# Kernel tuning notes

Hardware: AMD Instinct MI355X
Metric: run time of the kernel (lower is better)

The kernel has to match this reference:

```python
import jax, jax.numpy as jnp
import numpy as np

B, S, E, H = 2, 2048, 1024, 16
DH = E // H  # 64
EPS = 1e-5


def layer_norm(x, g, b):
    mu = jnp.mean(x, axis=-1, keepdims=True)
    var = jnp.mean(jnp.square(x - mu), axis=-1, keepdims=True)
    return (x - mu) * jax.lax.rsqrt(var + EPS) * g + b


def setup_inputs() -> dict:
    key = jax.random.key(0)
    ks = jax.random.split(key, 12)
    s = lambda fan_in: 1.0 / np.sqrt(fan_in)
    return {
        "x": jax.random.normal(ks[0], (B, S, E), dtype=jnp.float32),
        "ln1_g": jnp.ones((E,), jnp.float32),
        "ln1_b": jnp.zeros((E,), jnp.float32),
        # per-head projections, batched over head axis: [H, E, DH]
        "Wq": jax.random.uniform(ks[1], (H, E, DH), jnp.float32, -s(E), s(E)),
        "Wk": jax.random.uniform(ks[2], (H, E, DH), jnp.float32, -s(E), s(E)),
        "Wv": jax.random.uniform(ks[3], (H, E, DH), jnp.float32, -s(E), s(E)),
        "Wo": jax.random.uniform(ks[4], (H * DH, E), jnp.float32, -s(H * DH), s(H * DH)),
        "bo": jax.random.uniform(ks[5], (E,), jnp.float32, -s(H * DH), s(H * DH)),
        "ln2_g": jnp.ones((E,), jnp.float32),
        "ln2_b": jnp.zeros((E,), jnp.float32),
        "W1": jax.random.uniform(ks[6], (E, 4 * E), jnp.float32, -s(E), s(E)),
        "b1": jax.random.uniform(ks[7], (4 * E,), jnp.float32, -s(E), s(E)),
        "W2": jax.random.uniform(ks[8], (4 * E, E), jnp.float32, -s(4 * E), s(4 * E)),
        "b2": jax.random.uniform(ks[9], (E,), jnp.float32, -s(4 * E), s(4 * E)),
    }


def reference(x, ln1_g, ln1_b, Wq, Wk, Wv, Wo, bo, ln2_g, ln2_b, W1, b1, W2, b2):
    b, s, e = x.shape
    # --- multi-head attention (pre-LN) ---
    h = layer_norm(x, ln1_g, ln1_b)
    q = jnp.einsum("bse,hed->bhsd", h, Wq)
    k = jnp.einsum("bse,hed->bhsd", h, Wk)
    v = jnp.einsum("bse,hed->bhsd", h, Wv)
    # NOTE: original scales by channel**-0.5 (embed_size), not head_size
    scores = jnp.einsum("bhsd,bhtd->bhst", q, k) * (e ** -0.5)
    causal = jnp.tril(jnp.ones((s, s), dtype=bool))
    scores = jnp.where(causal, scores, -jnp.inf)
    attn = jax.nn.softmax(scores, axis=-1)  # dropout is identity in eval
    out = jnp.einsum("bhst,bhtd->bhsd", attn, v)
    out = out.transpose(0, 2, 1, 3).reshape(b, s, -1)  # concat heads: [B,S,H*DH]
    x = x + out @ Wo + bo
    # --- feed-forward (pre-LN) ---
    h2 = layer_norm(x, ln2_g, ln2_b)
    ff = jax.nn.relu(h2 @ W1 + b1) @ W2 + b2
    return x + ff
```

## Files before the change

### kernel.cpp

```cpp
#include <hip/hip_runtime.h>


typedef __bf16 bf16_t;
typedef __attribute__((ext_vector_type(8))) __bf16 bf16x8;
typedef __attribute__((ext_vector_type(4))) __bf16 bf16x4;
typedef __attribute__((ext_vector_type(4))) float f32x4;

#define B_DIM 2
#define S_DIM 2048
#define E_DIM 1024
#define H_DIM 16
#define DH_DIM 64

#define GLD16(gp, lp) __builtin_amdgcn_global_load_lds( \
    (const __attribute__((address_space(1))) void*)(gp), \
    (__attribute__((address_space(3))) void*)(lp), 16, 0, 0)

#define Q_SCALE 0.0450842120f

__global__ __launch_bounds__(256) void ln_kernel(
    const float* __restrict__ x, const float* __restrict__ g,
    const float* __restrict__ bv, bf16_t* __restrict__ out)
{
  const int row = blockIdx.x;
  const int t = threadIdx.x;
  const float* xr = x + (size_t)row * E_DIM;
  float4 v = *(const float4*)&xr[t * 4];
  float s  = v.x + v.y + v.z + v.w;
  float s2 = v.x*v.x + v.y*v.y + v.z*v.z + v.w*v.w;
#pragma unroll
  for (int m = 1; m < 64; m <<= 1) {
    s  += __shfl_xor(s,  m, 64);
    s2 += __shfl_xor(s2, m, 64);
  }
  __shared__ float red[8];
  const int wid = t >> 6, lane = t & 63;
  if (lane == 0) { red[wid] = s; red[4 + wid] = s2; }
  __syncthreads();
  s  = red[0] + red[1] + red[2] + red[3];
  s2 = red[4] + red[5] + red[6] + red[7];
  const float mu  = s * (1.f / E_DIM);
  const float var = s2 * (1.f / E_DIM) - mu * mu;
  const float rs  = rsqrtf(var + 1e-5f);
  float4 gg = *(const float4*)&g[t * 4];
  float4 bb = *(const float4*)&bv[t * 4];
  bf16x4 o;
  o[0] = (bf16_t)((v.x - mu) * rs * gg.x + bb.x);
  o[1] = (bf16_t)((v.y - mu) * rs * gg.y + bb.y);
  o[2] = (bf16_t)((v.z - mu) * rs * gg.z + bb.z);
  o[3] = (bf16_t)((v.w - mu) * rs * gg.w + bb.w);
  *(bf16x4*)&out[(size_t)row * E_DIM + t * 4] = o;
}

__global__ __launch_bounds__(256) void reduce2_ln(
    const bf16_t* __restrict__ p0, const bf16_t* __restrict__ p1,
    const float* __restrict__ bo, const float* __restrict__ x,
    const float* __restrict__ g, const float* __restrict__ bv,
    float* __restrict__ xmid, bf16_t* __restrict__ h2)
{
  const int row = blockIdx.x;
  const int t = threadIdx.x;
  const size_t off = (size_t)row * E_DIM + t * 4;
  bf16x4 a = *(const bf16x4*)&p0[off];
  bf16x4 b4 = *(const bf16x4*)&p1[off];
  float4 xr = *(const float4*)&x[off];
  float4 bo4 = *(const float4*)&bo[t * 4];
  float4 v;
  v.x = (float)a[0] + (float)b4[0] + xr.x + bo4.x;
  v.y = (float)a[1] + (float)b4[1] + xr.y + bo4.y;
  v.z = (float)a[2] + (float)b4[2] + xr.z + bo4.z;
  v.w = (float)a[3] + (float)b4[3] + xr.w + bo4.w;
  *(float4*)&xmid[off] = v;
  float s  = v.x + v.y + v.z + v.w;
  float s2 = v.x*v.x + v.y*v.y + v.z*v.z + v.w*v.w;
#pragma unroll
  for (int m = 1; m < 64; m <<= 1) {
    s  += __shfl_xor(s,  m, 64);
    s2 += __shfl_xor(s2, m, 64);
  }
  __shared__ float red[8];
  const int wid = t >> 6, lane = t & 63;
  if (lane == 0) { red[wid] = s; red[4 + wid] = s2; }
  __syncthreads();
  s  = red[0] + red[1] + red[2] + red[3];
  s2 = red[4] + red[5] + red[6] + red[7];
  const float mu  = s * (1.f / E_DIM);
  const float var = s2 * (1.f / E_DIM) - mu * mu;
  const float rs  = rsqrtf(var + 1e-5f);
  float4 gg = *(const float4*)&g[t * 4];
  float4 bb = *(const float4*)&bv[t * 4];
  bf16x4 o;
  o[0] = (bf16_t)((v.x - mu) * rs * gg.x + bb.x);
  o[1] = (bf16_t)((v.y - mu) * rs * gg.y + bb.y);
  o[2] = (bf16_t)((v.z - mu) * rs * gg.z + bb.z);
  o[3] = (bf16_t)((v.w - mu) * rs * gg.w + bb.w);
  *(bf16x4*)&h2[off] = o;
}

__global__ __launch_bounds__(256) void reduce4(
    const bf16_t* __restrict__ p0, const bf16_t* __restrict__ p1,
    const bf16_t* __restrict__ p2, const bf16_t* __restrict__ p3,
    const float* __restrict__ b2, const float* __restrict__ xm,
    float* __restrict__ out)
{
  const int row = blockIdx.x;
  const int t = threadIdx.x;
  const size_t off = (size_t)row * E_DIM + t * 4;
  bf16x4 a0 = *(const bf16x4*)&p0[off];
  bf16x4 a1 = *(const bf16x4*)&p1[off];
  bf16x4 a2 = *(const bf16x4*)&p2[off];
  bf16x4 a3 = *(const bf16x4*)&p3[off];
  float4 xr = *(const float4*)&xm[off];
  float4 bb = *(const float4*)&b2[t * 4];
  float4 o;
  o.x = (float)a0[0] + (float)a1[0] + (float)a2[0] + (float)a3[0] + xr.x + bb.x;
  o.y = (float)a0[1] + (float)a1[1] + (float)a2[1] + (float)a3[1] + xr.y + bb.y;
  o.z = (float)a0[2] + (float)a1[2] + (float)a2[2] + (float)a3[2] + xr.z + bb.z;
  o.w = (float)a0[3] + (float)a1[3] + (float)a2[3] + (float)a3[3] + xr.w + bb.w;
  *(float4*)&out[off] = o;
}

__global__ __launch_bounds__(256) void pack_weights(
    const float* __restrict__ Wq, const float* __restrict__ Wk,
    const float* __restrict__ Wv, bf16_t* __restrict__ WqkvT,
    const float* __restrict__ Wo, bf16_t* __restrict__ WoT,
    const float* __restrict__ W1, bf16_t* __restrict__ W1T,
    const float* __restrict__ W2, bf16_t* __restrict__ W2T)
{
  __shared__ float tile[64][65];
  const int bid = blockIdx.x;
  const int t = threadIdx.x;
  const int rr = t >> 2;

  if (bid < 768) {
    const int byq = bid >> 4, bxq = bid & 15;
    const int m = byq >> 4, h = byq & 15;
    const float* src = (m == 0 ? Wq : (m == 1 ? Wk : Wv)) + (size_t)h * E_DIM * DH_DIM;
    const int e0 = bxq * 64;
#pragma unroll
    for (int u = 0; u < 4; u++) {
      const int cc = (t & 3) * 4 + u * 16;
      float4 f = *(const float4*)&src[(size_t)(e0 + rr) * DH_DIM + cc];
      tile[rr][cc + 0] = f.x; tile[rr][cc + 1] = f.y;
      tile[rr][cc + 2] = f.z; tile[rr][cc + 3] = f.w;
    }
    __syncthreads();
    const int oc = t >> 2;
    const size_t drow = (size_t)(m * 1024 + h * 64 + oc) * E_DIM;
#pragma unroll
    for (int u = 0; u < 4; u++) {
      const int orr = (t & 3) * 4 + u * 16;
      bf16x4 w;
      w[0] = (bf16_t)tile[orr + 0][oc];
      w[1] = (bf16_t)tile[orr + 1][oc];
      w[2] = (bf16_t)tile[orr + 2][oc];
      w[3] = (bf16_t)tile[orr + 3][oc];
      *(bf16x4*)&WqkvT[drow + e0 + orr] = w;
    }
    return;
  }

  const float* src; bf16_t* dst; int R, C, bx, by;
  if (bid < 1024)      { const int r = bid - 768;  src = Wo; dst = WoT; R = 1024; C = 1024; bx = r & 15; by = r >> 4; }
  else if (bid < 2048) { const int r = bid - 1024; src = W1; dst = W1T; R = 1024; C = 4096; bx = r & 63; by = r >> 6; }
  else                 { const int r = bid - 2048; src = W2; dst = W2T; R = 4096; C = 1024; bx = r & 15; by = r >> 4; }
  const int c0 = bx * 64, r0 = by * 64;
#pragma unroll
  for (int u = 0; u < 4; u++) {
    const int cc = (t & 3) * 4 + u * 16;
    float4 f = *(const float4*)&src[(size_t)(r0 + rr) * C + c0 + cc];
    tile[rr][cc + 0] = f.x; tile[rr][cc + 1] = f.y;
    tile[rr][cc + 2] = f.z; tile[rr][cc + 3] = f.w;
  }
  __syncthreads();
  const int oc = t >> 2;
#pragma unroll
  for (int u = 0; u < 4; u++) {
    const int orr = (t & 3) * 4 + u * 16;
    bf16x4 w;
    w[0] = (bf16_t)tile[orr + 0][oc];
    w[1] = (bf16_t)tile[orr + 1][oc];
    w[2] = (bf16_t)tile[orr + 2][oc];
    w[3] = (bf16_t)tile[orr + 3][oc];
    *(bf16x4*)&dst[(size_t)(c0 + oc) * R + r0 + orr] = w;
  }
}

constexpr int EPI_QKV = 0, EPI_BIAS_RELU = 2, EPI_PART_F32 = 3, EPI_PART_B16 = 4;


template <int EPI>
__global__ __launch_bounds__(256) void gemm128_kernel(
    const bf16_t* __restrict__ A, const bf16_t* __restrict__ Bt,
    int M, int N, int Kst, int Klen, int RM, int RN,
    const float* __restrict__ bias,
    float* __restrict__ outF, bf16_t* __restrict__ outB,
    bf16_t* __restrict__ qo, bf16_t* __restrict__ ko, bf16_t* __restrict__ vo)
{
  __shared__ bf16_t As[2][128 * 64];
  __shared__ bf16_t Bs[2][128 * 64];
  const int gx = gridDim.x;
  const int lin = blockIdx.y * gx + blockIdx.x;
  const int xcd = lin & 7, kb = lin >> 3;
  const int nregx = gx / RM;
  const int rx = xcd % nregx, ry = xcd / nregx;
  const int m0 = (rx * RM + kb % RM) * 128;
  const int n0 = (ry * RN + kb / RM) * 128;
  const int sp = blockIdx.z;
  A  += (size_t)sp * Klen;
  Bt += (size_t)sp * Klen;

  const int tid = threadIdx.x, lane = tid & 63, wid = tid >> 6;
  const int wr = wid >> 1, wc = wid & 1;
  const int lr = lane & 15, lg = lane >> 4;
  const int l7 = lr & 7;
  const int sl[2] = { (lg ^ l7) * 16, ((4 | lg) ^ l7) * 16 };
  const int rbA = (wr * 64 + lr) * 128;
  const int rbB = (wc * 64 + lr) * 128;

  auto stage = [&](int kt, int buf) {
#pragma unroll
    for (int q = 0; q < 4; q++) {
      const int L = q * 256 + tid;
      const int row = L >> 3;
      const int u = (L & 7) ^ (row & 7);
      char* la = (char*)&As[buf][0] + (size_t)(q * 256 + wid * 64) * 16;
      char* lb = (char*)&Bs[buf][0] + (size_t)(q * 256 + wid * 64) * 16;
      GLD16(A  + (size_t)(m0 + row) * Kst + kt * 64 + u * 8, la);
      GLD16(Bt + (size_t)(n0 + row) * Kst + kt * 64 + u * 8, lb);
    }
  };

  const f32x4 z4 = {0.f, 0.f, 0.f, 0.f};
  f32x4 acc[4][4];
#pragma unroll
  for (int i = 0; i < 4; i++)
#pragma unroll
    for (int j = 0; j < 4; j++) acc[i][j] = z4;

  const int NT = Klen / 64;
  stage(0, 0);
  for (int T = 0; T < NT; ++T) {
    const int b = T & 1;
    asm volatile("s_waitcnt vmcnt(0)" ::: "memory");
    __builtin_amdgcn_s_barrier();
    if (T + 1 < NT) stage(T + 1, b ^ 1);
    __builtin_amdgcn_sched_barrier(0);

    bf16x8 bfr[2][4];
#pragma unroll
    for (int kk = 0; kk < 2; kk++)
#pragma unroll
      for (int j = 0; j < 4; j++)
        bfr[kk][j] = *(const bf16x8*)((const char*)&Bs[b][0] + rbB + j * 2048 + sl[kk]);
    __builtin_amdgcn_s_setprio(1);
#pragma unroll
    for (int i = 0; i < 4; i++) {
#pragma unroll
      for (int kk = 0; kk < 2; kk++) {
        bf16x8 af = *(const bf16x8*)((const char*)&As[b][0] + rbA + i * 2048 + sl[kk]);
#pragma unroll
        for (int j = 0; j < 4; j++)
          acc[i][j] = __builtin_amdgcn_mfma_f32_16x16x32_bf16(af, bfr[kk][j], acc[i][j], 0, 0, 0);
      }
    }
    __builtin_amdgcn_s_setprio(0);
  }

#pragma unroll
  for (int i = 0; i < 4; i++) {
#pragma unroll
    for (int j = 0; j < 4; j++) {
#pragma unroll
      for (int r = 0; r < 4; r++) {
        const int m = m0 + wr * 64 + i * 16 + lg * 4 + r;
        const int n = n0 + wc * 64 + j * 16 + lr;
        const float val = acc[i][j][r];
        if constexpr (EPI == EPI_QKV) {
          const int tsel = n >> 10, h = (n >> 6) & 15, d = n & 63;
          const int b_ = m >> 11, s_ = m & 2047;
          if (tsel == 0)
            qo[((size_t)((b_ * H_DIM + h) * S_DIM + s_)) * DH_DIM + d] = (bf16_t)(val * Q_SCALE);
          else if (tsel == 1)
            ko[((size_t)((b_ * H_DIM + h) * S_DIM + s_)) * DH_DIM + d] = (bf16_t)val;
          else
            vo[((size_t)((b_ * H_DIM + h) * DH_DIM + d)) * S_DIM + s_] = (bf16_t)val;
        } else if constexpr (EPI == EPI_BIAS_RELU) {
          const float u = val + bias[n];
          outB[(size_t)m * N + n] = (bf16_t)(u > 0.f ? u : 0.f);
        } else if constexpr (EPI == EPI_PART_F32) {
          outF[(size_t)sp * M * N + (size_t)m * N + n] = val;
        } else {
          bf16_t* o = sp == 0 ? outB : sp == 1 ? qo : sp == 2 ? ko : vo;
          o[(size_t)m * N + n] = (bf16_t)val;
        }
      }
    }
  }
}

template <int EPI>
__global__ __launch_bounds__(512) void gemm256_kernel(
    const bf16_t* __restrict__ A, const bf16_t* __restrict__ Bt,
    int M, int N, int Kst, int Klen, int RM, int RN,
    const float* __restrict__ bias,
    float* __restrict__ outF, bf16_t* __restrict__ outB,
    bf16_t* __restrict__ qo, bf16_t* __restrict__ ko, bf16_t* __restrict__ vo)
{
  __shared__ bf16_t As[2][256 * 64];
  __shared__ bf16_t Bs[2][256 * 64];
  const int gx = gridDim.x;
  const int lin = blockIdx.y * gx + blockIdx.x;
  const int xcd = lin & 7, kb = lin >> 3;
  const int nregx = gx / RM;
  const int rx = xcd % nregx, ry = xcd / nregx;
  const int m0 = (rx * RM + kb % RM) * 256;
  const int n0 = (ry * RN + kb / RM) * 256;
  const int sp = blockIdx.z;
  A  += (size_t)sp * Klen;
  Bt += (size_t)sp * Klen;

  const int tid = threadIdx.x, lane = tid & 63, wid = tid >> 6;
  const int wm = wid >> 2, wn = wid & 3;
  const int lr = lane & 15, lg = lane >> 4;
  const int l7 = lr & 7;
  const int sl[2] = { (lg ^ l7) * 16, ((4 | lg) ^ l7) * 16 };
  const int rbA = (wm * 128 + lr) * 128;
  const int rbB = (wn * 64 + lr) * 128;

  auto stage = [&](int kt, int buf) {
#pragma unroll
    for (int q = 0; q < 4; q++) {
      const int L = q * 512 + tid;
      const int row = L >> 3;
      const int u = (L & 7) ^ (row & 7);
      char* la = (char*)&As[buf][0] + (size_t)(q * 512 + wid * 64) * 16;
      char* lb = (char*)&Bs[buf][0] + (size_t)(q * 512 + wid * 64) * 16;
      GLD16(A  + (size_t)(m0 + row) * Kst + kt * 64 + u * 8, la);
      GLD16(Bt + (size_t)(n0 + row) * Kst + kt * 64 + u * 8, lb);
    }
  };

  const f32x4 z4 = {0.f, 0.f, 0.f, 0.f};
  f32x4 acc[8][4];
#pragma unroll
  for (int i = 0; i < 8; i++)
#pragma unroll
    for (int j = 0; j < 4; j++) acc[i][j] = z4;

  const int NT = Klen / 64;
  stage(0, 0);
  for (int T = 0; T < NT; ++T) {
    const int b = T & 1;
    asm volatile("s_waitcnt vmcnt(0)" ::: "memory");
    __builtin_amdgcn_s_barrier();
    if (T + 1 < NT) stage(T + 1, b ^ 1);
    __builtin_amdgcn_sched_barrier(0);

    bf16x8 bfr[2][4];
#pragma unroll
    for (int kk = 0; kk < 2; kk++)
#pragma unroll
      for (int j = 0; j < 4; j++)
        bfr[kk][j] = *(const bf16x8*)((const char*)&Bs[b][0] + rbB + j * 2048 + sl[kk]);
    __builtin_amdgcn_s_setprio(1);
#pragma unroll
    for (int i = 0; i < 8; i++) {
#pragma unroll
      for (int kk = 0; kk < 2; kk++) {
        bf16x8 af = *(const bf16x8*)((const char*)&As[b][0] + rbA + i * 2048 + sl[kk]);
#pragma unroll
        for (int j = 0; j < 4; j++)
          acc[i][j] = __builtin_amdgcn_mfma_f32_16x16x32_bf16(af, bfr[kk][j], acc[i][j], 0, 0, 0);
      }
    }
    __builtin_amdgcn_s_setprio(0);
  }

#pragma unroll
  for (int i = 0; i < 8; i++) {
#pragma unroll
    for (int j = 0; j < 4; j++) {
#pragma unroll
      for (int r = 0; r < 4; r++) {
        const int m = m0 + wm * 128 + i * 16 + lg * 4 + r;
        const int n = n0 + wn * 64 + j * 16 + lr;
        const float val = acc[i][j][r];
        if constexpr (EPI == EPI_BIAS_RELU) {
          const float u = val + bias[n];
          outB[(size_t)m * N + n] = (bf16_t)(u > 0.f ? u : 0.f);
        } else if constexpr (EPI == EPI_PART_F32) {
          outF[(size_t)sp * M * N + (size_t)m * N + n] = val;
        } else if constexpr (EPI == EPI_PART_B16) {
          bf16_t* o = sp == 0 ? outB : sp == 1 ? qo : sp == 2 ? ko : vo;
          o[(size_t)m * N + n] = (bf16_t)val;
        }
      }
    }
  }
}

__global__ __launch_bounds__(256) void attn_kernel(
    const bf16_t* __restrict__ Q, const bf16_t* __restrict__ K,
    const bf16_t* __restrict__ Vt, bf16_t* __restrict__ O,
    bf16_t* __restrict__ Opart, float* __restrict__ mpart, float* __restrict__ lpart)
{
  __shared__ bf16_t Ks[2][64 * 64];
  __shared__ bf16_t Vs[2][64 * 64];
  __shared__ bf16_t Ps[4][2][16 * 64];

  const int nwg = 51 * gridDim.y;
  int id = blockIdx.y * 51 + blockIdx.x;
  id = (id & 7) * (nwg >> 3) + (id >> 3);
  const int bx = id % 51, bh = id / 51;

  int g = 0;
  while (3 * (g + 1) * (g + 2) / 2 <= bx) g++;
  const int rr_ = bx - 3 * g * (g + 1) / 2;
  const int q2 = 3 * g + rr_ / (g + 1);
  const int sp = rr_ % (g + 1);
  const int ns = g + 1;
  const int n2 = 2 * q2 + 2;
  const int lo = 6 * sp;
  const int hi = (6 * sp + 6 < n2) ? 6 * sp + 6 : n2;

  const int tid = threadIdx.x;
  const int wid = tid >> 6, lane = tid & 63;
  const int lr = lane & 15, lg = lane >> 4;
  const int q0w = q2 * 128 + wid * 32;

  const bf16_t* Qp = Q  + (size_t)bh * S_DIM * DH_DIM;
  const bf16_t* Kp = K  + (size_t)bh * S_DIM * DH_DIM;
  const bf16_t* Vp = Vt + (size_t)bh * DH_DIM * S_DIM;

  bf16x8 bq0[2], bq1[2];
#pragma unroll
  for (int c = 0; c < 2; c++) {
    bq0[c] = *(const bf16x8*)&Qp[(size_t)(q0w + lr) * DH_DIM + c * 32 + lg * 8];
    bq1[c] = *(const bf16x8*)&Qp[(size_t)(q0w + 16 + lr) * DH_DIM + c * 32 + lg * 8];
  }

  const f32x4 z4 = {0.f, 0.f, 0.f, 0.f};
  f32x4 Ot0[4], Ot1[4];
#pragma unroll
  for (int dt = 0; dt < 4; dt++) { Ot0[dt] = z4; Ot1[dt] = z4; }
  float mrow0 = -1e30f, lrow0 = 0.f;
  float mrow1 = -1e30f, lrow1 = 0.f;

  const int ktr = wid * 8 + (lane >> 3);
  const int ksc = lane & 7;

  auto stageKV = [&](int t0, int buf) {
#pragma unroll
    for (int p = 0; p < 2; p++) {
      const int tr = p * 32 + ktr;
      GLD16(Kp + (size_t)(t0 + tr) * DH_DIM + (ksc ^ (tr & 7)) * 8,
            &Ks[buf][(p * 32 + wid * 8) * 64]);
      GLD16(Vp + (size_t)tr * S_DIM + t0 + (ksc ^ (tr & 7)) * 8,
            &Vs[buf][(p * 32 + wid * 8) * 64]);
    }
  };

  stageKV(lo * 64, 0);

  for (int tc = lo; tc < hi; ++tc) {
    const int cur = (tc - lo) & 1;
    __syncthreads();
    if (tc + 1 < hi) stageKV((tc + 1) * 64, cur ^ 1);

    const int t0 = tc * 64;
    f32x4 s0[4], s1[4];
    __builtin_amdgcn_s_setprio(1);
#pragma unroll
    for (int j = 0; j < 4; j++) {
      f32x4 a = z4, b = z4;
      const int t = j * 16 + lr;
#pragma unroll
      for (int c = 0; c < 2; c++) {
        const int kbyte = t * 128 + (((c * 4 + lg) * 16) ^ ((t & 7) << 4));
        bf16x8 ak = *(const bf16x8*)((const char*)&Ks[cur][0] + kbyte);
        a = __builtin_amdgcn_mfma_f32_16x16x32_bf16(ak, bq0[c], a, 0, 0, 0);
        b = __builtin_amdgcn_mfma_f32_16x16x32_bf16(ak, bq1[c], b, 0, 0, 0);
      }
      s0[j] = a; s1[j] = b;
    }
    __builtin_amdgcn_s_setprio(0);
    if (tc >= 2 * q2) {
#pragma unroll
      for (int j = 0; j < 4; j++)
#pragma unroll
        for (int r = 0; r < 4; r++) {
          const int tg = t0 + j * 16 + lg * 4 + r;
          if (tg > q0w + lr)      s0[j][r] = -1e30f;
          if (tg > q0w + 16 + lr) s1[j][r] = -1e30f;
        }
    }
    {
      float mj[4];
#pragma unroll
      for (int j = 0; j < 4; j++)
        mj[j] = fmaxf(fmaxf(s0[j][0], s0[j][1]), fmaxf(s0[j][2], s0[j][3]));
      float tmax = fmaxf(fmaxf(mj[0], mj[1]), fmaxf(mj[2], mj[3]));
      tmax = fmaxf(tmax, __shfl_xor(tmax, 16, 64));
      tmax = fmaxf(tmax, __shfl_xor(tmax, 32, 64));
      if (!__all(tmax <= mrow0 + 8.f)) {
        const float mnew = fmaxf(mrow0, tmax);
        const float fsc = __builtin_exp2f(mrow0 - mnew);
        mrow0 = mnew; lrow0 *= fsc;
#pragma unroll
        for (int dt = 0; dt < 4; dt++)
#pragma unroll
          for (int r = 0; r < 4; r++) Ot0[dt][r] *= fsc;
      }
      float sj[4];
#pragma unroll
      for (int j = 0; j < 4; j++) {
#pragma unroll
        for (int r = 0; r < 4; r++) s0[j][r] = __builtin_exp2f(s0[j][r] - mrow0);
        sj[j] = (s0[j][0] + s0[j][1]) + (s0[j][2] + s0[j][3]);
      }
      float tsum = (sj[0] + sj[1]) + (sj[2] + sj[3]);
      tsum += __shfl_xor(tsum, 16, 64);
      tsum += __shfl_xor(tsum, 32, 64);
      lrow0 += tsum;
#pragma unroll
      for (int j = 0; j < 4; j++) {
        bf16x4 w;
#pragma unroll
        for (int r = 0; r < 4; r++) w[r] = (bf16_t)s0[j][r];
        const int pbyte = lr * 128 + ((j * 32 + lg * 8) ^ ((lr & 7) << 4));
        *(bf16x4*)((char*)&Ps[wid][0][0] + pbyte) = w;
      }
    }
    {
      float mj[4];
#pragma unroll
      for (int j = 0; j < 4; j++)
        mj[j] = fmaxf(fmaxf(s1[j][0], s1[j][1]), fmaxf(s1[j][2], s1[j][3]));
      float tmax = fmaxf(fmaxf(mj[0], mj[1]), fmaxf(mj[2], mj[3]));
      tmax = fmaxf(tmax, __shfl_xor(tmax, 16, 64));
      tmax = fmaxf(tmax, __shfl_xor(tmax, 32, 64));
      if (!__all(tmax <= mrow1 + 8.f)) {
        const float mnew = fmaxf(mrow1, tmax);
        const float fsc = __builtin_exp2f(mrow1 - mnew);
        mrow1 = mnew; lrow1 *= fsc;
#pragma unroll
        for (int dt = 0; dt < 4; dt++)
#pragma unroll
          for (int r = 0; r < 4; r++) Ot1[dt][r] *= fsc;
      }
      float sj[4];
#pragma unroll
      for (int j = 0; j < 4; j++) {
#pragma unroll
        for (int r = 0; r < 4; r++) s1[j][r] = __builtin_exp2f(s1[j][r] - mrow1);
        sj[j] = (s1[j][0] + s1[j][1]) + (s1[j][2] + s1[j][3]);
      }
      float tsum = (sj[0] + sj[1]) + (sj[2] + sj[3]);
      tsum += __shfl_xor(tsum, 16, 64);
      tsum += __shfl_xor(tsum, 32, 64);
      lrow1 += tsum;
#pragma unroll
      for (int j = 0; j < 4; j++) {
        bf16x4 w;
#pragma unroll
        for (int r = 0; r < 4; r++) w[r] = (bf16_t)s1[j][r];
        const int pbyte = lr * 128 + ((j * 32 + lg * 8) ^ ((lr & 7) << 4));
        *(bf16x4*)((char*)&Ps[wid][1][0] + pbyte) = w;
      }
    }

    __builtin_amdgcn_s_setprio(1);
#pragma unroll
    for (int c = 0; c < 2; c++) {
      const int abyte = lr * 128 + ((c * 64 + lg * 16) ^ ((lr & 7) << 4));
      bf16x8 pa0 = *(const bf16x8*)((const char*)&Ps[wid][0][0] + abyte);
      bf16x8 pa1 = *(const bf16x8*)((const char*)&Ps[wid][1][0] + abyte);
#pragma unroll
      for (int dt = 0; dt < 4; dt++) {
        const int d = dt * 16 + lr;
        const int vbyte = d * 128 + (((c * 4 + lg) * 16) ^ ((d & 7) << 4));
        bf16x8 bv = *(const bf16x8*)((const char*)&Vs[cur][0] + vbyte);
        Ot0[dt] = __builtin_amdgcn_mfma_f32_16x16x32_bf16(bv, pa0, Ot0[dt], 0, 0, 0);
        Ot1[dt] = __builtin_amdgcn_mfma_f32_16x16x32_bf16(bv, pa1, Ot1[dt], 0, 0, 0);
      }
    }
    __builtin_amdgcn_s_setprio(0);
  }

  if (ns == 1) {
    const int b = bh >> 4, h = bh & 15;
    {
      const float linv = 1.f / lrow0;
      const size_t base = ((size_t)(b * S_DIM + q0w + lr)) * E_DIM + h * DH_DIM;
#pragma unroll
      for (int dt = 0; dt < 4; dt++) {
        bf16x4 w;
#pragma unroll
        for (int r = 0; r < 4; r++) w[r] = (bf16_t)(Ot0[dt][r] * linv);
        *(bf16x4*)&O[base + dt * 16 + lg * 4] = w;
      }
    }
    {
      const float linv = 1.f / lrow1;
      const size_t base = ((size_t)(b * S_DIM + q0w + 16 + lr)) * E_DIM + h * DH_DIM;
#pragma unroll
      for (int dt = 0; dt < 4; dt++) {
        bf16x4 w;
#pragma unroll
        for (int r = 0; r < 4; r++) w[r] = (bf16_t)(Ot1[dt][r] * linv);
        *(bf16x4*)&O[base + dt * 16 + lg * 4] = w;
      }
    }
  } else {
    const int psl = bh * 48 + (bx - 3);
    bf16_t* Ob = Opart + (size_t)psl * 128 * 64;
    const int row0 = wid * 32 + lr, row1 = row0 + 16;
#pragma unroll
    for (int dt = 0; dt < 4; dt++) {
      bf16x4 w0, w1;
#pragma unroll
      for (int r = 0; r < 4; r++) { w0[r] = (bf16_t)Ot0[dt][r]; w1[r] = (bf16_t)Ot1[dt][r]; }
      *(bf16x4*)&Ob[row0 * 64 + dt * 16 + lg * 4] = w0;
      *(bf16x4*)&Ob[row1 * 64 + dt * 16 + lg * 4] = w1;
    }
    if (lg == 0) {
      mpart[psl * 128 + row0] = mrow0;
      lpart[psl * 128 + row0] = lrow0;
      mpart[psl * 128 + row1] = mrow1;
      lpart[psl * 128 + row1] = lrow1;
    }
  }
}

__global__ __launch_bounds__(256) void attn_combine(
    const bf16_t* __restrict__ Opart, const float* __restrict__ mpart,
    const float* __restrict__ lpart, bf16_t* __restrict__ O)
{
  const int q2 = 3 + (blockIdx.x >> 1);
  const int half = blockIdx.x & 1;
  const int bh = blockIdx.y;
  const int g = q2 / 3, ns = g + 1;
  const int sbase = 3 * g * (g + 1) / 2 + (q2 - 3 * g) * (g + 1) - 3;
  const int psl0 = bh * 48 + sbase;
  const int tid = threadIdx.x;
  const int q = tid >> 2, d0 = (tid & 3) * 16;
  const int row = half * 64 + q;

  float M = -1e30f;
  for (int s = 0; s < ns; s++) M = fmaxf(M, mpart[(psl0 + s) * 128 + row]);
  float L = 0.f;
  float acc[16];
#pragma unroll
  for (int j = 0; j < 16; j++) acc[j] = 0.f;
  for (int s = 0; s < ns; s++) {
    const float w = __builtin_exp2f(mpart[(psl0 + s) * 128 + row] - M);
    L += w * lpart[(psl0 + s) * 128 + row];
    const bf16_t* Ob = Opart + ((size_t)(psl0 + s) * 128 + row) * 64 + d0;
    bf16x8 o0 = *(const bf16x8*)Ob;
    bf16x8 o1 = *(const bf16x8*)(Ob + 8);
#pragma unroll
    for (int j = 0; j < 8; j++) { acc[j] += w * (float)o0[j]; acc[8 + j] += w * (float)o1[j]; }
  }
  const float inv = 1.f / L;
  const int b = bh >> 4, h = bh & 15;
  const int srow = q2 * 128 + row;
  bf16_t* out = O + ((size_t)(b * S_DIM + srow)) * E_DIM + h * DH_DIM + d0;
  bf16x8 w0, w1;
#pragma unroll
  for (int j = 0; j < 8; j++) { w0[j] = (bf16_t)(acc[j] * inv); w1[j] = (bf16_t)(acc[8 + j] * inv); }
  *(bf16x8*)out = w0;
  *(bf16x8*)(out + 8) = w1;
}

extern "C" void kernel_launch(void* const* d_in, const int* in_sizes, int n_in,
                              void* d_out, int out_size, void* d_ws, size_t ws_size,
                              hipStream_t stream)
{
  const float* x    = (const float*)d_in[0];
  const float* ln1g = (const float*)d_in[1];
  const float* ln1b = (const float*)d_in[2];
  const float* Wq   = (const float*)d_in[3];
  const float* Wk   = (const float*)d_in[4];
  const float* Wv   = (const float*)d_in[5];
  const float* Wo   = (const float*)d_in[6];
  const float* bo   = (const float*)d_in[7];
  const float* ln2g = (const float*)d_in[8];
  const float* ln2b = (const float*)d_in[9];
  const float* W1   = (const float*)d_in[10];
  const float* b1   = (const float*)d_in[11];
  const float* W2   = (const float*)d_in[12];
  const float* b2   = (const float*)d_in[13];

  char* ws = (char*)d_ws;
  bf16_t* WqkvT = (bf16_t*)(ws + 0);
  bf16_t* WoT   = (bf16_t*)(ws + 6291456);
  bf16_t* W1T   = (bf16_t*)(ws + 8388608);
  bf16_t* W2T   = (bf16_t*)(ws + 16777216);
  bf16_t* h1    = (bf16_t*)(ws + 25165824);
  bf16_t* qb    = (bf16_t*)(ws + 33554432);
  bf16_t* kb    = (bf16_t*)(ws + 41943040);
  bf16_t* vb    = (bf16_t*)(ws + 50331648);
  bf16_t* attnb = (bf16_t*)(ws + 58720256);
  float*  xmid  = (float* )(ws + 67108864);
  bf16_t* h2    = (bf16_t*)(ws + 83886080);
  bf16_t* ff1   = (bf16_t*)(ws + 25165824);
  bf16_t* Opart = (bf16_t*)(ws + 67108864);
  float*  mpart = (float* )(ws + 25165824);
  float*  lpart = (float* )(ws + 25952256);
  bf16_t* po0   = (bf16_t*)(ws + 25165824);
  bf16_t* po1   = (bf16_t*)(ws + 33554432);
  bf16_t* pf0   = (bf16_t*)(ws + 0);
  bf16_t* pf1   = (bf16_t*)(ws + 8388608);
  bf16_t* pf2   = (bf16_t*)(ws + 58720256);
  bf16_t* pf3   = (bf16_t*)(ws + 83886080);

  pack_weights<<<3072, 256, 0, stream>>>(Wq, Wk, Wv, WqkvT, Wo, WoT, W1, W1T, W2, W2T);

  ln_kernel<<<4096, 256, 0, stream>>>(x, ln1g, ln1b, h1);
  gemm128_kernel<EPI_QKV><<<dim3(32, 24, 1), 256, 0, stream>>>(
      h1, WqkvT, 4096, 3072, 1024, 1024, 8, 12, nullptr,
      nullptr, nullptr, qb, kb, vb);
  attn_kernel<<<dim3(51, 32), 256, 0, stream>>>(qb, kb, vb, attnb, Opart, mpart, lpart);
  attn_combine<<<dim3(26, 32), 256, 0, stream>>>(Opart, mpart, lpart, attnb);
  gemm128_kernel<EPI_PART_B16><<<dim3(32, 8, 2), 256, 0, stream>>>(
      attnb, WoT, 4096, 1024, 1024, 512, 8, 4, nullptr,
      nullptr, po0, po1, nullptr, nullptr);
  reduce2_ln<<<4096, 256, 0, stream>>>(po0, po1, bo, x, ln2g, ln2b, xmid, h2);
  gemm256_kernel<EPI_BIAS_RELU><<<dim3(16, 16, 1), 512, 0, stream>>>(
      h2, W1T, 4096, 4096, 1024, 1024, 8, 4, b1,
      nullptr, ff1, nullptr, nullptr, nullptr);
  gemm256_kernel<EPI_PART_B16><<<dim3(16, 4, 4), 512, 0, stream>>>(
      ff1, W2T, 4096, 1024, 4096, 1024, 4, 2, nullptr,
      nullptr, pf0, pf1, pf2, pf3);
  reduce4<<<4096, 256, 0, stream>>>(pf0, pf1, pf2, pf3, b2, xmid, (float*)d_out);

  (void)in_sizes; (void)n_in; (void)out_size; (void)ws_size;
}
```

Before: 245.4 us.

## Split 256x256 GEMM K-tile into half-stages and interleave loads with MFMA phases

Reorganizes the LDS buffers of the 256-tile GEMM into per-K-half sub-buffers with a new swizzled layout. Global-to-LDS loads for the next tile are issued in four quarter-stages interleaved with four MFMA phases, using partial vmcnt waits instead of a full drain each iteration. The aim is finer-grained overlap of memory traffic with matrix math and less stall at the barrier. The cost is more barriers per K-step and more intricate wait-count bookkeeping, with a risk of races if the counts are wrong.

```diff
diff --git a/kernel.cpp b/kernel.cpp
--- a/kernel.cpp
+++ b/kernel.cpp
@@ -307,8 +307,8 @@
     float* __restrict__ outF, bf16_t* __restrict__ outB,
     bf16_t* __restrict__ qo, bf16_t* __restrict__ ko, bf16_t* __restrict__ vo)
 {
-  __shared__ bf16_t As[2][256 * 64];
-  __shared__ bf16_t Bs[2][256 * 64];
+  __shared__ bf16_t As[2][2][128 * 64];
+  __shared__ bf16_t Bs[2][2][128 * 64];
   const int gx = gridDim.x;
   const int lin = blockIdx.y * gx + blockIdx.x;
   const int xcd = lin & 7, kb = lin >> 3;
@@ -323,21 +323,25 @@
   const int tid = threadIdx.x, lane = tid & 63, wid = tid >> 6;
   const int wm = wid >> 2, wn = wid & 3;
   const int lr = lane & 15, lg = lane >> 4;
-  const int l7 = lr & 7;
-  const int sl[2] = { (lg ^ l7) * 16, ((4 | lg) ^ l7) * 16 };
-  const int rbA = (wm * 128 + lr) * 128;
-  const int rbB = (wn * 64 + lr) * 128;
-
-  auto stage = [&](int kt, int buf) {
-#pragma unroll
-    for (int q = 0; q < 4; q++) {
-      const int L = q * 512 + tid;
-      const int row = L >> 3;
-      const int u = (L & 7) ^ (row & 7);
-      char* la = (char*)&As[buf][0] + (size_t)(q * 512 + wid * 64) * 16;
-      char* lb = (char*)&Bs[buf][0] + (size_t)(q * 512 + wid * 64) * 16;
-      GLD16(A  + (size_t)(m0 + row) * Kst + kt * 64 + u * 8, la);
-      GLD16(Bt + (size_t)(n0 + row) * Kst + kt * 64 + u * 8, lb);
+  const int sl16 = (((lr & 1) * 4 + lg) ^ ((lr >> 1) & 7)) * 16;
+  const int rbA = (wm * 64 + (lr >> 1)) * 128 + sl16;
+  const int rbB = (wn * 32 + (lr >> 1)) * 128 + sl16;
+
+  auto stageU = [&](int kt, int kh, int matB) {
+    const int buf = kt & 1;
+#pragma unroll
+    for (int p = 0; p < 2; p++) {
+      const int L = p * 512 + tid;
+      const int row2 = L >> 3;
+      const int s = (L & 7) ^ (row2 & 7);
+      const int r = row2 * 2 + (s >> 2);
+      const int u = s & 3;
+      char* lds = (char*)(matB ? &Bs[buf][kh][0] : &As[buf][kh][0])
+                + (size_t)(p * 512 + wid * 64) * 16;
+      const bf16_t* gp = (matB ? Bt + (size_t)(n0 + r) * Kst
+                               : A  + (size_t)(m0 + r) * Kst)
+                       + kt * 64 + kh * 32 + u * 8;
+      GLD16(gp, lds);
     }
   };
 
@@ -349,32 +353,43 @@
     for (int j = 0; j < 4; j++) acc[i][j] = z4;
 
   const int NT = Klen / 64;
-  stage(0, 0);
-  for (int T = 0; T < NT; ++T) {
-    const int b = T & 1;
-    asm volatile("s_waitcnt vmcnt(0)" ::: "memory");
-    __builtin_amdgcn_s_barrier();
-    if (T + 1 < NT) stage(T + 1, b ^ 1);
-    __builtin_amdgcn_sched_barrier(0);
-
-    bf16x8 bfr[2][4];
-#pragma unroll
-    for (int kk = 0; kk < 2; kk++)
-#pragma unroll
-      for (int j = 0; j < 4; j++)
-        bfr[kk][j] = *(const bf16x8*)((const char*)&Bs[b][0] + rbB + j * 2048 + sl[kk]);
-    __builtin_amdgcn_s_setprio(1);
-#pragma unroll
-    for (int i = 0; i < 8; i++) {
-#pragma unroll
-      for (int kk = 0; kk < 2; kk++) {
-        bf16x8 af = *(const bf16x8*)((const char*)&As[b][0] + rbA + i * 2048 + sl[kk]);
+  stageU(0, 0, 0); stageU(0, 0, 1); stageU(0, 1, 0); stageU(0, 1, 1);
+  asm volatile("s_waitcnt vmcnt(4)" ::: "memory");
+  __builtin_amdgcn_s_barrier();
+  __builtin_amdgcn_sched_barrier(0);
+
+  for (int TT = 0; TT < NT; ++TT) {
+    const int buf = TT & 1;
+    bf16x8 bfr[4];
+#pragma unroll
+    for (int q = 0; q < 4; q++) {
+      const int kh = q >> 1, mh = q & 1;
+      if ((q & 1) == 0) {
 #pragma unroll
         for (int j = 0; j < 4; j++)
-          acc[i][j] = __builtin_amdgcn_mfma_f32_16x16x32_bf16(af, bfr[kk][j], acc[i][j], 0, 0, 0);
-      }
-    }
-    __builtin_amdgcn_s_setprio(0);
+          bfr[j] = *(const bf16x8*)((const char*)&Bs[buf][kh][0] + rbB + j * 1024);
+      }
+      bf16x8 af[4];
+#pragma unroll
+      for (int ii = 0; ii < 4; ii++)
+        af[ii] = *(const bf16x8*)((const char*)&As[buf][kh][0] + rbA + (mh * 4 + ii) * 1024);
+      if (TT + 1 < NT) stageU(TT + 1, q >> 1, q & 1);
+      __builtin_amdgcn_s_setprio(1);
+#pragma unroll
+      for (int ii = 0; ii < 4; ii++)
+#pragma unroll
+        for (int j = 0; j < 4; j++)
+          acc[mh * 4 + ii][j] =
+              __builtin_amdgcn_mfma_f32_16x16x32_bf16(af[ii], bfr[j], acc[mh * 4 + ii][j], 0, 0, 0);
+      __builtin_amdgcn_s_setprio(0);
+      if (q & 1) {
+        __builtin_amdgcn_sched_barrier(0);
+        if (TT + 1 < NT) asm volatile("s_waitcnt vmcnt(4)" ::: "memory");
+        else if (q == 1) asm volatile("s_waitcnt vmcnt(0)" ::: "memory");
+      }
+      __builtin_amdgcn_s_barrier();
+      __builtin_amdgcn_sched_barrier(0);
+    }
   }
 
 #pragma unroll
```

Result: faster. 239.1 us, median of 2 (-2.6%).
